# Kernel tuning notes

Hardware: AMD Instinct MI355X
Metric: run time of the kernel (lower is better)

The kernel has to match this reference:

```python
import jax, jax.numpy as jnp
import numpy as np

N = 100000   # nodes
E = 1600000  # edges
F_IN = 128
H = 128
C = 40


def setup_inputs() -> dict:
    key = jax.random.key(0)
    ks = jax.random.split(key, 8)
    s = 0.05
    return {
        "x": jax.random.normal(ks[0], (N, F_IN), dtype=jnp.float32),
        "edge_index": jax.random.randint(ks[1], (2, E), 0, N, dtype=jnp.int32),
        "W1": jax.random.normal(ks[2], (F_IN, H), dtype=jnp.float32) * s,
        "b1": jnp.zeros((H,), jnp.float32),
        "W2": jax.random.normal(ks[3], (H, H), dtype=jnp.float32) * s,
        "b2": jnp.zeros((H,), jnp.float32),
        "Wfc": jax.random.normal(ks[4], (H, C), dtype=jnp.float32) * s,
        "bfc": jnp.zeros((C,), jnp.float32),
    }


def _graph_conv(x, src, dst, norm_out, norm_in, W, b):
    # DGL GraphConv, norm='both': h = D_in^{-1/2} A D_out^{-1/2} x W + b
    h = (x * norm_out[:, None]) @ W                      # [N, H] (W first: in>=out)
    agg = jax.ops.segment_sum(h[src], dst, num_segments=N)  # gather + scatter-add
    return agg * norm_in[:, None] + b


def reference(x, edge_index, W1, b1, W2, b2, Wfc, bfc):
    src, dst = edge_index[0], edge_index[1]
    ones = jnp.ones((E,), x.dtype)
    deg_out = jnp.maximum(jax.ops.segment_sum(ones, src, num_segments=N), 1.0)
    deg_in = jnp.maximum(jax.ops.segment_sum(ones, dst, num_segments=N), 1.0)
    norm_out = jax.lax.rsqrt(deg_out)
    norm_in = jax.lax.rsqrt(deg_in)
    # layer 0: GraphConv + relu (dropout is identity in eval mode)
    h = jax.nn.relu(_graph_conv(x, src, dst, norm_out, norm_in, W1, b1))
    # layer 1: GraphConv, no activation
    h = _graph_conv(h, src, dst, norm_out, norm_in, W2, b2)
    # final FC
    return h @ Wfc + bfc
```

## Files before the change

### kernel.cpp

```cpp
#include <hip/hip_runtime.h>
#include <hip/hip_fp16.h>


#define CHUNK    4096
#define NBK      800
#define SLAB     3072

typedef __attribute__((ext_vector_type(8))) short bf16x8;
typedef __attribute__((ext_vector_type(4))) float f32x4;

struct __align__(8)  half4 { __half x, y, z, w; };
struct __align__(16) half8 { __half h[8]; };

__device__ __forceinline__ unsigned short f2bf(float f) {
    union { float f; unsigned u; } v; v.f = f;
    unsigned r = v.u + 0x7FFFu + ((v.u >> 16) & 1u);
    return (unsigned short)(r >> 16);
}
__device__ __forceinline__ float bf2f(unsigned short h) {
    union { unsigned u; float f; } v; v.u = ((unsigned)h) << 16;
    return v.f;
}

__global__ void setup_kernel(const float* __restrict__ W1, const float* __restrict__ W2,
                             const float* __restrict__ Wfc,
                             const float* __restrict__ b2, const float* __restrict__ bfc,
                             unsigned short* __restrict__ Wh1, unsigned short* __restrict__ Wl1,
                             unsigned short* __restrict__ Wh2, unsigned short* __restrict__ Wl2,
                             float* __restrict__ b2p,
                             int* __restrict__ cur_d, int* __restrict__ cur_s, int nbuck) {
    int idx = blockIdx.x * blockDim.x + threadIdx.x;
    if (idx < nbuck) { cur_d[idx] = idx * SLAB; cur_s[idx] = idx * SLAB; }

    if (idx < 16384) {
        int k = idx >> 7, nn = idx & 127;
        float v = W1[idx];
        int q = k >> 5, j = k & 7, lb = ((k >> 3) & 3) * 16;
        int tcol = nn >> 4;
        int l = lb + (nn & 15);
        int pos = ((tcol * 4 + q) * 64 + l) * 8 + j;
        unsigned short h = f2bf(v);
        Wh1[pos] = h;
        Wl1[pos] = f2bf(v - bf2f(h));
    } else if (idx < 16384 + 6144) {
        int i2 = idx - 16384;
        int k = i2 / 48, nn = i2 - k * 48;
        float v = 0.f;
        if (nn < 40) {
            const float* w2row = W2 + k * 128;
            #pragma unroll 8
            for (int jj = 0; jj < 128; ++jj) v += w2row[jj] * Wfc[jj * 40 + nn];
        }
        int t = nn >> 4, q = k >> 5, j = k & 7;
        int l = ((k >> 3) & 3) * 16 + (nn & 15);
        int pos = ((t * 4 + q) * 64 + l) * 8 + j;
        unsigned short h = f2bf(v);
        Wh2[pos] = h;
        Wl2[pos] = f2bf(v - bf2f(h));
    } else if (idx < 16384 + 6144 + 40) {
        int c = idx - (16384 + 6144);
        float a = bfc[c];
        #pragma unroll 8
        for (int j = 0; j < 128; ++j) a += b2[j] * Wfc[j * 40 + c];
        b2p[c] = a;
    }
}

__global__ __launch_bounds__(256) void scatter_res_kernel(
        const int* __restrict__ src, const int* __restrict__ dst,
        int* __restrict__ cur_d, int* __restrict__ cur_s,
        unsigned int* __restrict__ ppack, unsigned char* __restrict__ es_loc,
        int E) {
    __shared__ int hd[NBK], hs[NBK], bd[NBK], bs[NBK];
    const int tid = threadIdx.x;
    for (int i = tid; i < NBK; i += 256) { hd[i] = 0; hs[i] = 0; }
    __syncthreads();
    const int base = blockIdx.x * CHUNK;
    const int end  = min(base + CHUNK, E);
    for (int e = base + tid; e < end; e += 256) {
        atomicAdd(&hd[((unsigned)dst[e]) >> 7], 1);
        atomicAdd(&hs[((unsigned)src[e]) >> 7], 1);
    }
    __syncthreads();
    for (int i = tid; i < NBK; i += 256) {
        int cd = hd[i];
        bd[i] = cd ? atomicAdd(&cur_d[i], cd) : 0;
        hd[i] = 0;
        int cs = hs[i];
        bs[i] = cs ? atomicAdd(&cur_s[i], cs) : 0;
        hs[i] = 0;
    }
    __syncthreads();
    for (int e = base + tid; e < end; e += 256) {
        int d = dst[e], s = src[e];
        unsigned bin_d = ((unsigned)d) >> 7;
        int pos = bd[bin_d] + atomicAdd(&hd[bin_d], 1);
        ppack[pos] = (((unsigned)d & 127u) << 17) | (unsigned)s;
        unsigned bin_s = ((unsigned)s) >> 7;
        int ps = bs[bin_s] + atomicAdd(&hs[bin_s], 1);
        es_loc[ps] = (unsigned char)(s & 127);
    }
}

__global__ __launch_bounds__(256) void fine_kernel(
        const unsigned int* __restrict__ ppack, const int* __restrict__ cur_d,
        const unsigned char* __restrict__ es_loc, const int* __restrict__ cur_s,
        int* __restrict__ deg_in, float* __restrict__ norm_in,
        int* __restrict__ row_ptr, int* __restrict__ csr_src,
        float* __restrict__ norm_out, int N_) {
    __shared__ int h[128];
    __shared__ int psum[128];
    const int tid = threadIdx.x;
    const int b = blockIdx.x;
    const int start = b * SLAB;
    const int node  = (b << 7) + tid;

    const int end_d = cur_d[b];
    if (tid < 128) h[tid] = 0;
    __syncthreads();
    for (int i = start + tid; i < end_d; i += 256)
        atomicAdd(&h[ppack[i] >> 17], 1);
    __syncthreads();

    int a = 0;
    if (tid < 128) { a = h[tid]; psum[tid] = a; }
    __syncthreads();
    for (int off = 1; off < 128; off <<= 1) {
        int t = 0;
        if (tid < 128 && tid >= off) t = psum[tid - off];
        __syncthreads();
        if (tid < 128) psum[tid] += t;
        __syncthreads();
    }

    if (tid < 128) {
        int base0 = psum[tid] - a + start;
        if (node < N_) {
            deg_in[node]  = a;
            row_ptr[node] = base0;
            norm_in[node] = rsqrtf((float)(a < 1 ? 1 : a));
        }
        h[tid] = base0;
    }
    __syncthreads();

    for (int i = start + tid; i < end_d; i += 256) {
        unsigned int pk = ppack[i];
        int pos = atomicAdd(&h[pk >> 17], 1);
        csr_src[pos] = (int)(pk & 0x1FFFFu);
    }
    __syncthreads();

    const int end_s = cur_s[b];
    if (tid < 128) h[tid] = 0;
    __syncthreads();
    for (int i = start + tid; i < end_s; i += 256)
        atomicAdd(&h[(int)es_loc[i]], 1);
    __syncthreads();

    if (tid < 128 && node < N_) {
        int d = h[tid];
        norm_out[node] = rsqrtf((float)(d < 1 ? 1 : d));
    }
}

__global__ __launch_bounds__(256, 3) void gemm128(
        const float* __restrict__ X, const float* __restrict__ scale,
        const unsigned short* __restrict__ Wh, const unsigned short* __restrict__ Wl,
        __half* __restrict__ Y, int nrows) {
    const int tid  = threadIdx.x;
    const int lane = tid & 63;
    const int w    = tid >> 6;
    const int m    = lane & 15;
    const int quad = lane >> 4;
    const int rowBase = blockIdx.x * 128 + w * 32;

    bf16x8 Ah[2][4], Al[2][4];
    #pragma unroll
    for (int rt = 0; rt < 2; ++rt) {
        int r = rowBase + rt * 16 + m;
        float sc = (r < nrows) ? scale[r] : 0.f;
        const float* xr = X + (size_t)(r < nrows ? r : 0) * 128;
        #pragma unroll
        for (int q = 0; q < 4; ++q) {
            int k0 = q * 32 + quad * 8;
            float4 a = *(const float4*)(xr + k0);
            float4 bv = *(const float4*)(xr + k0 + 4);
            float v[8] = {a.x * sc, a.y * sc, a.z * sc, a.w * sc,
                          bv.x * sc, bv.y * sc, bv.z * sc, bv.w * sc};
            bf16x8 hi, lo;
            #pragma unroll
            for (int j = 0; j < 8; ++j) {
                unsigned short h = f2bf(v[j]);
                hi[j] = (short)h;
                lo[j] = (short)f2bf(v[j] - bf2f(h));
            }
            Ah[rt][q] = hi; Al[rt][q] = lo;
        }
    }

    f32x4 acc[2][8];
    #pragma unroll
    for (int rt = 0; rt < 2; ++rt)
        #pragma unroll
        for (int t = 0; t < 8; ++t)
            acc[rt][t] = (f32x4){0.f, 0.f, 0.f, 0.f};

    #pragma unroll
    for (int t = 0; t < 8; ++t) {
        #pragma unroll
        for (int q = 0; q < 4; ++q) {
            const int off = ((t * 4 + q) * 64 + lane) * 8;
            bf16x8 Bh = *(const bf16x8*)(Wh + off);
            bf16x8 Bl = *(const bf16x8*)(Wl + off);
            #pragma unroll
            for (int rt = 0; rt < 2; ++rt) {
                acc[rt][t] = __builtin_amdgcn_mfma_f32_16x16x32_bf16(Ah[rt][q], Bh, acc[rt][t], 0, 0, 0);
                acc[rt][t] = __builtin_amdgcn_mfma_f32_16x16x32_bf16(Ah[rt][q], Bl, acc[rt][t], 0, 0, 0);
                acc[rt][t] = __builtin_amdgcn_mfma_f32_16x16x32_bf16(Al[rt][q], Bh, acc[rt][t], 0, 0, 0);
            }
        }
    }

    #pragma unroll
    for (int rt = 0; rt < 2; ++rt) {
        int r0 = rowBase + rt * 16 + quad * 4;
        #pragma unroll
        for (int reg = 0; reg < 4; ++reg) {
            int r = r0 + reg;
            if (r >= nrows) continue;
            __half* yr = Y + (size_t)r * 128 + m;
            #pragma unroll
            for (int t = 0; t < 8; ++t)
                yr[t * 16] = __float2half(acc[rt][t][reg]);
        }
    }
}

__global__ __launch_bounds__(256, 4) void gemm40(
        const __half* __restrict__ H, const float* __restrict__ scale,
        const unsigned short* __restrict__ Wh, const unsigned short* __restrict__ Wl,
        __half* __restrict__ G, int n) {
    const int tid  = threadIdx.x;
    const int lane = tid & 63;
    const int w    = tid >> 6;
    const int m    = lane & 15;
    const int quad = lane >> 4;
    const int rowBase = blockIdx.x * 128 + w * 32;

    bf16x8 Ah[2][4], Al[2][4];
    #pragma unroll
    for (int rt = 0; rt < 2; ++rt) {
        int r = rowBase + rt * 16 + m;
        float sc = (r < n) ? scale[r] : 0.f;
        const __half* xr = H + (size_t)(r < n ? r : 0) * 128;
        #pragma unroll
        for (int q = 0; q < 4; ++q) {
            int k0 = q * 32 + quad * 8;
            half4 a = *(const half4*)(xr + k0);
            half4 bv = *(const half4*)(xr + k0 + 4);
            float v[8] = {__half2float(a.x) * sc, __half2float(a.y) * sc,
                          __half2float(a.z) * sc, __half2float(a.w) * sc,
                          __half2float(bv.x) * sc, __half2float(bv.y) * sc,
                          __half2float(bv.z) * sc, __half2float(bv.w) * sc};
            bf16x8 hi, lo;
            #pragma unroll
            for (int j = 0; j < 8; ++j) {
                unsigned short h = f2bf(v[j]);
                hi[j] = (short)h;
                lo[j] = (short)f2bf(v[j] - bf2f(h));
            }
            Ah[rt][q] = hi; Al[rt][q] = lo;
        }
    }

    f32x4 acc[2][3];
    #pragma unroll
    for (int rt = 0; rt < 2; ++rt)
        #pragma unroll
        for (int t = 0; t < 3; ++t)
            acc[rt][t] = (f32x4){0.f, 0.f, 0.f, 0.f};

    #pragma unroll
    for (int t = 0; t < 3; ++t) {
        #pragma unroll
        for (int q = 0; q < 4; ++q) {
            const int off = ((t * 4 + q) * 64 + lane) * 8;
            bf16x8 Bh = *(const bf16x8*)(Wh + off);
            bf16x8 Bl = *(const bf16x8*)(Wl + off);
            #pragma unroll
            for (int rt = 0; rt < 2; ++rt) {
                acc[rt][t] = __builtin_amdgcn_mfma_f32_16x16x32_bf16(Ah[rt][q], Bh, acc[rt][t], 0, 0, 0);
                acc[rt][t] = __builtin_amdgcn_mfma_f32_16x16x32_bf16(Ah[rt][q], Bl, acc[rt][t], 0, 0, 0);
                acc[rt][t] = __builtin_amdgcn_mfma_f32_16x16x32_bf16(Al[rt][q], Bh, acc[rt][t], 0, 0, 0);
            }
        }
    }

    #pragma unroll
    for (int rt = 0; rt < 2; ++rt) {
        int r0 = rowBase + rt * 16 + quad * 4;
        #pragma unroll
        for (int reg = 0; reg < 4; ++reg) {
            int r = r0 + reg;
            if (r >= n) continue;
            __half* gr = G + (size_t)r * 64;
            #pragma unroll
            for (int t = 0; t < 3; ++t) {
                int col = t * 16 + m;
                if (col < 40) gr[col] = __float2half(acc[rt][t][reg]);
            }
        }
    }
}

__global__ __launch_bounds__(256) void gather_kernel(
        const __half* __restrict__ H, const int* __restrict__ row_ptr,
        const int* __restrict__ deg, const int* __restrict__ csr_src,
        const float* __restrict__ norm_in, const float* __restrict__ b,
        __half* __restrict__ out, int n) {
    const int tid  = threadIdx.x;
    const int node = blockIdx.x * 16 + (tid >> 4);
    const int c    = (tid & 15) * 8;
    if (node >= n) return;

    const int start = row_ptr[node];
    const int cnt   = deg[node];
    float acc[8] = {0.f, 0.f, 0.f, 0.f, 0.f, 0.f, 0.f, 0.f};

    int j = 0;
    for (; j + 4 <= cnt; j += 4) {
        int s0 = csr_src[start + j];
        int s1 = csr_src[start + j + 1];
        int s2 = csr_src[start + j + 2];
        int s3 = csr_src[start + j + 3];
        half8 v0 = *(const half8*)(H + (long long)s0 * 128 + c);
        half8 v1 = *(const half8*)(H + (long long)s1 * 128 + c);
        half8 v2 = *(const half8*)(H + (long long)s2 * 128 + c);
        half8 v3 = *(const half8*)(H + (long long)s3 * 128 + c);
        #pragma unroll
        for (int k = 0; k < 8; ++k)
            acc[k] += (__half2float(v0.h[k]) + __half2float(v1.h[k]))
                    + (__half2float(v2.h[k]) + __half2float(v3.h[k]));
    }
    for (; j < cnt; ++j) {
        int s0 = csr_src[start + j];
        half8 v0 = *(const half8*)(H + (long long)s0 * 128 + c);
        #pragma unroll
        for (int k = 0; k < 8; ++k) acc[k] += __half2float(v0.h[k]);
    }

    float ni = norm_in[node];
    float4 b0 = *(const float4*)(b + c);
    float4 b1v = *(const float4*)(b + c + 4);
    half8 o;
    o.h[0] = __float2half(fmaxf(acc[0] * ni + b0.x, 0.f));
    o.h[1] = __float2half(fmaxf(acc[1] * ni + b0.y, 0.f));
    o.h[2] = __float2half(fmaxf(acc[2] * ni + b0.z, 0.f));
    o.h[3] = __float2half(fmaxf(acc[3] * ni + b0.w, 0.f));
    o.h[4] = __float2half(fmaxf(acc[4] * ni + b1v.x, 0.f));
    o.h[5] = __float2half(fmaxf(acc[5] * ni + b1v.y, 0.f));
    o.h[6] = __float2half(fmaxf(acc[6] * ni + b1v.z, 0.f));
    o.h[7] = __float2half(fmaxf(acc[7] * ni + b1v.w, 0.f));
    *(half8*)(out + (long long)node * 128 + c) = o;
}

__global__ __launch_bounds__(256) void gather40_kernel(
        const __half* __restrict__ G, const int* __restrict__ row_ptr,
        const int* __restrict__ deg, const int* __restrict__ csr_src,
        const float* __restrict__ norm_in, const float* __restrict__ b2p,
        float* __restrict__ out, int n) {
    const int t = blockIdx.x * 256 + threadIdx.x;
    if (t >= n * 5) return;
    const int node = t / 5;
    const int c    = (t - node * 5) * 8;

    const int start = row_ptr[node];
    const int cnt   = deg[node];
    float acc[8] = {0.f, 0.f, 0.f, 0.f, 0.f, 0.f, 0.f, 0.f};

    int j = 0;
    for (; j + 4 <= cnt; j += 4) {
        int s0 = csr_src[start + j];
        int s1 = csr_src[start + j + 1];
        int s2 = csr_src[start + j + 2];
        int s3 = csr_src[start + j + 3];
        half8 v0 = *(const half8*)(G + (long long)s0 * 64 + c);
        half8 v1 = *(const half8*)(G + (long long)s1 * 64 + c);
        half8 v2 = *(const half8*)(G + (long long)s2 * 64 + c);
        half8 v3 = *(const half8*)(G + (long long)s3 * 64 + c);
        #pragma unroll
        for (int k = 0; k < 8; ++k)
            acc[k] += (__half2float(v0.h[k]) + __half2float(v1.h[k]))
                    + (__half2float(v2.h[k]) + __half2float(v3.h[k]));
    }
    for (; j < cnt; ++j) {
        int s0 = csr_src[start + j];
        half8 v0 = *(const half8*)(G + (long long)s0 * 64 + c);
        #pragma unroll
        for (int k = 0; k < 8; ++k) acc[k] += __half2float(v0.h[k]);
    }

    float ni = norm_in[node];
    float4 o0, o1;
    o0.x = acc[0] * ni + b2p[c + 0];
    o0.y = acc[1] * ni + b2p[c + 1];
    o0.z = acc[2] * ni + b2p[c + 2];
    o0.w = acc[3] * ni + b2p[c + 3];
    o1.x = acc[4] * ni + b2p[c + 4];
    o1.y = acc[5] * ni + b2p[c + 5];
    o1.z = acc[6] * ni + b2p[c + 6];
    o1.w = acc[7] * ni + b2p[c + 7];
    float* op = out + (long long)node * 40 + c;
    *(float4*)(op)     = o0;
    *(float4*)(op + 4) = o1;
}

extern "C" void kernel_launch(void* const* d_in, const int* in_sizes, int n_in,
                              void* d_out, int out_size, void* d_ws, size_t ws_size,
                              hipStream_t stream) {
    const float* x   = (const float*)d_in[0];
    const int*   ei  = (const int*)  d_in[1];
    const float* W1  = (const float*)d_in[2];
    const float* b1  = (const float*)d_in[3];
    const float* W2  = (const float*)d_in[4];
    const float* b2  = (const float*)d_in[5];
    const float* Wfc = (const float*)d_in[6];
    const float* bfc = (const float*)d_in[7];
    float* out = (float*)d_out;

    const int N = in_sizes[0] / 128;
    const int E = in_sizes[1] / 2;
    const int* src = ei;
    const int* dst = ei + E;

    const int nbuck = (N + 127) >> 7;
    const int B1 = (E + CHUNK - 1) / CHUNK;

    char* p = (char*)d_ws;
    float* norm_out = (float*)p; p += (size_t)N * 4;
    float* norm_in  = (float*)p; p += (size_t)N * 4;
    float* bufA     = (float*)p; p += (size_t)N * 128 * 4;
    float* bufB     = (float*)p; p += (size_t)N * 128 * 4;
    int*   deg_in   = (int*)p;   p += (size_t)N * 4;
    int*   row_ptr  = (int*)p;   p += (size_t)N * 4;
    int*   csr_src  = (int*)p;   p += (size_t)NBK * SLAB * 4;
    int*   cur_d    = (int*)p;   p += (size_t)1024 * 4;
    int*   cur_s    = (int*)p;   p += (size_t)1024 * 4;
    float* b2p      = (float*)p; p += (size_t)64 * 4;
    unsigned short* Wh1 = (unsigned short*)p; p += (size_t)16384 * 2;
    unsigned short* Wl1 = (unsigned short*)p; p += (size_t)16384 * 2;
    unsigned short* Wh2 = (unsigned short*)p; p += (size_t)6144 * 2;
    unsigned short* Wl2 = (unsigned short*)p; p += (size_t)6144 * 2;

    unsigned int*  ppack  = (unsigned int*)bufB;
    unsigned char* es_loc = (unsigned char*)(ppack + (size_t)NBK * SLAB);

    __half* h1pre = (__half*)bufA;
    __half* G     = (__half*)bufA;
    __half* h1    = (__half*)bufB;

    const int T = 256;

    setup_kernel<<<(16384 + 6144 + 40 + T - 1) / T, T, 0, stream>>>(
        W1, W2, Wfc, b2, bfc, Wh1, Wl1, Wh2, Wl2, b2p, cur_d, cur_s, nbuck);
    scatter_res_kernel<<<B1, T, 0, stream>>>(src, dst, cur_d, cur_s, ppack, es_loc, E);
    fine_kernel<<<nbuck, T, 0, stream>>>(ppack, cur_d, es_loc, cur_s,
                                         deg_in, norm_in, row_ptr, csr_src,
                                         norm_out, N);

    const int gemm_grid = (N + 127) / 128;
    gemm128<<<gemm_grid, T, 0, stream>>>(x, norm_out, Wh1, Wl1, h1pre, N);
    const int gather_grid = (N + 15) / 16;
    gather_kernel<<<gather_grid, T, 0, stream>>>(h1pre, row_ptr, deg_in, csr_src,
                                                 norm_in, b1, h1, N);
    gemm40<<<gemm_grid, T, 0, stream>>>(h1, norm_out, Wh2, Wl2, G, N);
    gather40_kernel<<<((size_t)N * 5 + T - 1) / T, T, 0, stream>>>(
        G, row_ptr, deg_in, csr_src, norm_in, b2p, out, N);
}
```

Baseline: 290.0 us.

## Fuse layer-1 aggregation with the second 40-column GEMM via shared memory

```diff
diff --git a/kernel.cpp b/kernel.cpp
--- a/kernel.cpp
+++ b/kernel.cpp
@@ -237,95 +237,23 @@
     }
 }
 
-__global__ __launch_bounds__(256, 4) void gemm40(
-        const __half* __restrict__ H, const float* __restrict__ scale,
-        const unsigned short* __restrict__ Wh, const unsigned short* __restrict__ Wl,
-        __half* __restrict__ G, int n) {
-    const int tid  = threadIdx.x;
-    const int lane = tid & 63;
-    const int w    = tid >> 6;
-    const int m    = lane & 15;
-    const int quad = lane >> 4;
-    const int rowBase = blockIdx.x * 128 + w * 32;
-
-    bf16x8 Ah[2][4], Al[2][4];
-    #pragma unroll
-    for (int rt = 0; rt < 2; ++rt) {
-        int r = rowBase + rt * 16 + m;
-        float sc = (r < n) ? scale[r] : 0.f;
-        const __half* xr = H + (size_t)(r < n ? r : 0) * 128;
-        #pragma unroll
-        for (int q = 0; q < 4; ++q) {
-            int k0 = q * 32 + quad * 8;
-            half4 a = *(const half4*)(xr + k0);
-            half4 bv = *(const half4*)(xr + k0 + 4);
-            float v[8] = {__half2float(a.x) * sc, __half2float(a.y) * sc,
-                          __half2float(a.z) * sc, __half2float(a.w) * sc,
-                          __half2float(bv.x) * sc, __half2float(bv.y) * sc,
-                          __half2float(bv.z) * sc, __half2float(bv.w) * sc};
-            bf16x8 hi, lo;
-            #pragma unroll
-            for (int j = 0; j < 8; ++j) {
-                unsigned short h = f2bf(v[j]);
-                hi[j] = (short)h;
-                lo[j] = (short)f2bf(v[j] - bf2f(h));
-            }
-            Ah[rt][q] = hi; Al[rt][q] = lo;
-        }
-    }
-
-    f32x4 acc[2][3];
-    #pragma unroll
-    for (int rt = 0; rt < 2; ++rt)
-        #pragma unroll
-        for (int t = 0; t < 3; ++t)
-            acc[rt][t] = (f32x4){0.f, 0.f, 0.f, 0.f};
-
-    #pragma unroll
-    for (int t = 0; t < 3; ++t) {
-        #pragma unroll
-        for (int q = 0; q < 4; ++q) {
-            const int off = ((t * 4 + q) * 64 + lane) * 8;
-            bf16x8 Bh = *(const bf16x8*)(Wh + off);
-            bf16x8 Bl = *(const bf16x8*)(Wl + off);
-            #pragma unroll
-            for (int rt = 0; rt < 2; ++rt) {
-                acc[rt][t] = __builtin_amdgcn_mfma_f32_16x16x32_bf16(Ah[rt][q], Bh, acc[rt][t], 0, 0, 0);
-                acc[rt][t] = __builtin_amdgcn_mfma_f32_16x16x32_bf16(Ah[rt][q], Bl, acc[rt][t], 0, 0, 0);
-                acc[rt][t] = __builtin_amdgcn_mfma_f32_16x16x32_bf16(Al[rt][q], Bh, acc[rt][t], 0, 0, 0);
-            }
-        }
-    }
-
-    #pragma unroll
-    for (int rt = 0; rt < 2; ++rt) {
-        int r0 = rowBase + rt * 16 + quad * 4;
-        #pragma unroll
-        for (int reg = 0; reg < 4; ++reg) {
-            int r = r0 + reg;
-            if (r >= n) continue;
-            __half* gr = G + (size_t)r * 64;
-            #pragma unroll
-            for (int t = 0; t < 3; ++t) {
-                int col = t * 16 + m;
-                if (col < 40) gr[col] = __float2half(acc[rt][t][reg]);
-            }
-        }
-    }
-}
-
-__global__ __launch_bounds__(256) void gather_kernel(
+__global__ __launch_bounds__(256, 4) void gather_kernel(
         const __half* __restrict__ H, const int* __restrict__ row_ptr,
         const int* __restrict__ deg, const int* __restrict__ csr_src,
         const float* __restrict__ norm_in, const float* __restrict__ b,
-        __half* __restrict__ out, int n) {
-    const int tid  = threadIdx.x;
-    const int node = blockIdx.x * 16 + (tid >> 4);
-    const int c    = (tid & 15) * 8;
-    if (node >= n) return;
-
-    const int start = row_ptr[node];
-    const int cnt   = deg[node];
+        const float* __restrict__ norm_out,
+        const unsigned short* __restrict__ Wh2, const unsigned short* __restrict__ Wl2,
+        __half* __restrict__ G, int n) {
+    __shared__ float h1s[16][132];
+    const int tid   = threadIdx.x;
+    const int node0 = blockIdx.x * 16;
+    const int g     = tid >> 4;
+    const int node  = node0 + g;
+    const int c     = (tid & 15) * 8;
+    const bool active = node < n;
+
+    int start = 0, cnt = 0;
+    if (active) { start = row_ptr[node]; cnt = deg[node]; }
     float acc[8] = {0.f, 0.f, 0.f, 0.f, 0.f, 0.f, 0.f, 0.f};
 
     int j = 0;
@@ -350,19 +278,63 @@
         for (int k = 0; k < 8; ++k) acc[k] += __half2float(v0.h[k]);
     }
 
-    float ni = norm_in[node];
-    float4 b0 = *(const float4*)(b + c);
+    float ni = active ? norm_in[node] : 0.f;
+    float4 b0  = *(const float4*)(b + c);
     float4 b1v = *(const float4*)(b + c + 4);
-    half8 o;
-    o.h[0] = __float2half(fmaxf(acc[0] * ni + b0.x, 0.f));
-    o.h[1] = __float2half(fmaxf(acc[1] * ni + b0.y, 0.f));
-    o.h[2] = __float2half(fmaxf(acc[2] * ni + b0.z, 0.f));
-    o.h[3] = __float2half(fmaxf(acc[3] * ni + b0.w, 0.f));
-    o.h[4] = __float2half(fmaxf(acc[4] * ni + b1v.x, 0.f));
-    o.h[5] = __float2half(fmaxf(acc[5] * ni + b1v.y, 0.f));
-    o.h[6] = __float2half(fmaxf(acc[6] * ni + b1v.z, 0.f));
-    o.h[7] = __float2half(fmaxf(acc[7] * ni + b1v.w, 0.f));
-    *(half8*)(out + (long long)node * 128 + c) = o;
+    float bb[8] = {b0.x, b0.y, b0.z, b0.w, b1v.x, b1v.y, b1v.z, b1v.w};
+    #pragma unroll
+    for (int k = 0; k < 8; ++k)
+        h1s[g][c + k] = active ? fmaxf(acc[k] * ni + bb[k], 0.f) : 0.f;
+    __syncthreads();
+
+    const int w = tid >> 6;
+    if (w < 3) {
+        const int lane = tid & 63;
+        const int m    = lane & 15;
+        const int quad = lane >> 4;
+        const int r_a  = node0 + m;
+        const float sc = (r_a < n) ? norm_out[r_a] : 0.f;
+
+        bf16x8 Ah[4], Al[4];
+        #pragma unroll
+        for (int q = 0; q < 4; ++q) {
+            int k0 = q * 32 + quad * 8;
+            const float4* hp = (const float4*)&h1s[m][k0];
+            float4 va = hp[0], vb = hp[1];
+            float v[8] = {va.x * sc, va.y * sc, va.z * sc, va.w * sc,
+                          vb.x * sc, vb.y * sc, vb.z * sc, vb.w * sc};
+            bf16x8 hi, lo;
+            #pragma unroll
+            for (int jj = 0; jj < 8; ++jj) {
+                unsigned short h = f2bf(v[jj]);
+                hi[jj] = (short)h;
+                lo[jj] = (short)f2bf(v[jj] - bf2f(h));
+            }
+            Ah[q] = hi; Al[q] = lo;
+        }
+
+        f32x4 a3 = (f32x4){0.f, 0.f, 0.f, 0.f};
+        const int t = w;
+        #pragma unroll
+        for (int q = 0; q < 4; ++q) {
+            const int off = ((t * 4 + q) * 64 + lane) * 8;
+            bf16x8 Bh = *(const bf16x8*)(Wh2 + off);
+            bf16x8 Bl = *(const bf16x8*)(Wl2 + off);
+            a3 = __builtin_amdgcn_mfma_f32_16x16x32_bf16(Ah[q], Bh, a3, 0, 0, 0);
+            a3 = __builtin_amdgcn_mfma_f32_16x16x32_bf16(Ah[q], Bl, a3, 0, 0, 0);
+            a3 = __builtin_amdgcn_mfma_f32_16x16x32_bf16(Al[q], Bh, a3, 0, 0, 0);
+        }
+
+        const int col = t * 16 + m;
+        if (col < 40) {
+            const int r0 = node0 + quad * 4;
+            #pragma unroll
+            for (int reg = 0; reg < 4; ++reg) {
+                int r = r0 + reg;
+                if (r < n) G[(size_t)r * 64 + col] = __float2half(a3[reg]);
+            }
+        }
+    }
 }
 
 __global__ __launch_bounds__(256) void gather40_kernel(
@@ -457,8 +429,7 @@
     unsigned char* es_loc = (unsigned char*)(ppack + (size_t)NBK * SLAB);
 
     __half* h1pre = (__half*)bufA;
-    __half* G     = (__half*)bufA;
-    __half* h1    = (__half*)bufB;
+    __half* G     = (__half*)bufB;
 
     const int T = 256;
 
@@ -473,8 +444,8 @@
     gemm128<<<gemm_grid, T, 0, stream>>>(x, norm_out, Wh1, Wl1, h1pre, N);
     const int gather_grid = (N + 15) / 16;
     gather_kernel<<<gather_grid, T, 0, stream>>>(h1pre, row_ptr, deg_in, csr_src,
-                                                 norm_in, b1, h1, N);
-    gemm40<<<gemm_grid, T, 0, stream>>>(h1, norm_out, Wh2, Wl2, G, N);
+                                                 norm_in, b1, norm_out,
+                                                 Wh2, Wl2, G, N);
     gather40_kernel<<<((size_t)N * 5 + T - 1) / T, T, 0, stream>>>(
         G, row_ptr, deg_in, csr_src, norm_in, b2p, out, N);
 }
```

Result: faster. 279.1 us (-3.7%).
